# Kernel optimization log

Measured on AMD Instinct MI355X. Metric: run time of the kernel, lower is better.

## Reference

```python
import jax, jax.numpy as jnp
import numpy as np

HID = 1024     # hidden_dim
HEADS = 8      # num_heads
HD = HID // HEADS  # head_dim = 128
MD = 8         # manifold_dim
L = 3          # num_layers
B, S = 8, 1024
EPS = 1e-7
BALL_MAX = 1.0 - 1e-5  # clamp inside Poincare ball (|curvature| = 1)


def expmap0(v):
    """Hyperbolic exponential map at origin, curvature -1 (Poincare ball)."""
    n = jnp.sqrt(jnp.sum(v * v, axis=-1, keepdims=True))
    n = jnp.maximum(n, EPS)
    return jnp.tanh(n) * v / n


def logmap0(y):
    """Hyperbolic logarithm map at origin, curvature -1 (Poincare ball)."""
    n = jnp.sqrt(jnp.sum(y * y, axis=-1, keepdims=True))
    n_c = jnp.clip(n, EPS, BALL_MAX)
    return jnp.arctanh(n_c) * y / n_c


def setup_inputs() -> dict:
    key = jax.random.key(0)
    ks = jax.random.split(key, 6)
    sc = 0.02
    return {
        "x": jax.random.normal(ks[0], (B, S, HID), dtype=jnp.float32),
        "W_qkv": jax.random.normal(ks[1], (HID, 3 * HID), dtype=jnp.float32) * sc,
        "b_qkv": jnp.zeros((3 * HID,), dtype=jnp.float32),
        "W_pinv": jax.random.normal(ks[2], (HID, MD), dtype=jnp.float32) * sc,
        "b_pinv": jnp.zeros((MD,), dtype=jnp.float32),
        "W_attn": jax.random.normal(ks[3], (L, MD, HID), dtype=jnp.float32) * sc,
        "b_attn": jnp.zeros((L, HID), dtype=jnp.float32),
        "W_out": jax.random.normal(ks[4], (HID, HID), dtype=jnp.float32) * sc,
        "b_out": jnp.zeros((HID,), dtype=jnp.float32),
    }


def reference(x, W_qkv, b_qkv, W_pinv, b_pinv, W_attn, b_attn, W_out, b_out):
    inv_sqrt_d = 1.0 / np.sqrt(HD).astype(np.float32)
    cur = x
    for l in range(L):
        qkv = jnp.einsum('bsh,hd->bsd', cur, W_qkv) + b_qkv  # [B,S,3*HID]
        q, k, v = jnp.split(qkv, 3, axis=-1)
        # [B,S,HID] -> [B,HEADS,S,HD]
        def heads(t):
            return t.reshape(B, S, HEADS, HD).transpose(0, 2, 1, 3)
        q, k, v = heads(q), heads(k), heads(v)
        # geometric 'flow': hyperbolic retraction of Q/K onto the Poincare ball
        # (parallel transport at the origin is identity)
        qf = expmap0(q)
        kf = expmap0(k)
        scores = jnp.einsum('bhqd,bhkd->bhqk', qf, kf) * inv_sqrt_d
        att = jax.nn.softmax(scores, axis=-1)
        o = jnp.einsum('bhqk,bhkd->bhqd', att, v)  # [B,H,S,HD]
        o = o.transpose(0, 2, 1, 3).reshape(B, S, HID)
        # project to manifold coords, then per-layer pattern projection back
        m = jnp.einsum('bsh,hm->bsm', o, W_pinv) + b_pinv           # [B,S,MD]
        upd = jnp.einsum('bsm,mh->bsh', m, W_attn[l]) + b_attn[l]   # [B,S,HID]
        cur = cur + upd
    return jnp.einsum('bsh,hd->bsd', cur, W_out) + b_out
```

## Files before the change

### kernel.cpp

```cpp
#include <hip/hip_runtime.h>
#include <hip/hip_bf16.h>
#include <hip/hip_fp8.h>
#include <cstdint>

typedef __hip_bfloat16 bf16;
typedef __bf16 b8 __attribute__((ext_vector_type(8)));
typedef float f4v __attribute__((ext_vector_type(4)));
typedef short s8v __attribute__((ext_vector_type(8)));
typedef int i8v __attribute__((ext_vector_type(8)));

#define DEVI static __device__ __forceinline__

DEVI void gload16(const void* g, void* l) {
  __builtin_amdgcn_global_load_lds(
      (const __attribute__((address_space(1))) void*)(uintptr_t)g,
      (__attribute__((address_space(3))) void*)(uint32_t)(uintptr_t)l,
      16, 0, 0);
}

DEVI f4v mfma_bf16(b8 a, b8 b, f4v c) {
  return __builtin_amdgcn_mfma_f32_16x16x32_bf16(a, b, c, 0, 0, 0);
}

DEVI f4v mfma_fp8(i8v a, i8v b, f4v c) {
  return __builtin_amdgcn_mfma_scale_f32_16x16x128_f8f6f4(
      a, b, c, 0, 0, 0, 0x7F7F7F7F, 0, 0x7F7F7F7F);
}

DEVI uint8_t to_fp8(float f) {
  __hip_fp8_e4m3 v(f);
  return v.__x;
}

__global__ void prep_kernel(const float* __restrict__ x, float* __restrict__ cur,
                            bf16* __restrict__ curb, uint8_t* __restrict__ curf8) {
  int i = (blockIdx.x * 256 + threadIdx.x) * 4;
  float4 v = *(const float4*)(x + i);
  *(float4*)(cur + i) = v;
  __hip_bfloat162 a, b;
  a.x = __float2bfloat16(v.x); a.y = __float2bfloat16(v.y);
  b.x = __float2bfloat16(v.z); b.y = __float2bfloat16(v.w);
  *(__hip_bfloat162*)(curb + i) = a;
  *(__hip_bfloat162*)(curb + i + 2) = b;
  uint32_t p = (uint32_t)to_fp8(v.x) | ((uint32_t)to_fp8(v.y) << 8) |
               ((uint32_t)to_fp8(v.z) << 16) | ((uint32_t)to_fp8(v.w) << 24);
  *(uint32_t*)(curf8 + i) = p;
}

__global__ void transpose_cast(const float* __restrict__ in, bf16* __restrict__ out,
                               int R, int C) {
  __shared__ float tile[32][33];
  int c0 = blockIdx.x * 32, r0 = blockIdx.y * 32;
  int tx = threadIdx.x & 31, ty = threadIdx.x >> 5;
  for (int rr = ty; rr < 32; rr += 8)
    tile[rr][tx] = in[(size_t)(r0 + rr) * C + c0 + tx];
  __syncthreads();
  for (int cc = ty; cc < 32; cc += 8)
    out[(size_t)(c0 + cc) * R + r0 + tx] = __float2bfloat16(tile[tx][cc]);
}

__global__ void transpose_cast_fp8(const float* __restrict__ in,
                                   uint8_t* __restrict__ out, int R, int C) {
  __shared__ float tile[32][33];
  int c0 = blockIdx.x * 32, r0 = blockIdx.y * 32;
  int tx = threadIdx.x & 31, ty = threadIdx.x >> 5;
  for (int rr = ty; rr < 32; rr += 8)
    tile[rr][tx] = in[(size_t)(r0 + rr) * C + c0 + tx];
  __syncthreads();
  for (int cc = ty; cc < 32; cc += 8)
    out[(size_t)(c0 + cc) * R + r0 + tx] = to_fp8(tile[tx][cc]);
}

__global__ __launch_bounds__(256, 3)
void gemm_qkv_fp8(const uint8_t* __restrict__ A, const uint8_t* __restrict__ Bt,
                  const float* __restrict__ bias, bf16* __restrict__ Qo,
                  bf16* __restrict__ Ko, bf16* __restrict__ Vto, int M, int N,
                  int K) {
  __shared__ uint8_t As[128 * 128];
  __shared__ uint8_t Bs[128 * 128];
  __shared__ float red[2][128];
  const int t = threadIdx.x;
  const int w = t >> 6, lane = t & 63;
  const int lm = lane & 15, qd = lane >> 4;
  const int m0 = blockIdx.x * 128, n0 = blockIdx.y * 128;
  const int wm = (w & 1) * 64, wn = (w >> 1) * 64;

  const uint8_t* Ag = A + (size_t)m0 * K;
  const uint8_t* Bg = Bt + (size_t)n0 * K;

  f4v acc[4][4];
  f4v zero = {0.f, 0.f, 0.f, 0.f};
#pragma unroll
  for (int i = 0; i < 4; i++)
#pragma unroll
    for (int j = 0; j < 4; j++) acc[i][j] = zero;

  for (int k0 = 0; k0 < K; k0 += 128) {
#pragma unroll
    for (int c = 0; c < 4; c++) {
      int s = c * 256 + t;
      int r = s >> 3;
      int kc = (s & 7) ^ (r & 7);
      gload16(Ag + (size_t)r * K + k0 + kc * 16, &As[s * 16]);
      gload16(Bg + (size_t)r * K + k0 + kc * 16, &Bs[s * 16]);
    }
    __syncthreads();
    i8v af[4], bfr[4];
#pragma unroll
    for (int tm = 0; tm < 4; tm++) {
      int row = wm + tm * 16 + lm;
      int ch = (qd * 2) ^ (row & 7);
      union { int4 q[2]; i8v v; } u;
      u.q[0] = *(const int4*)&As[row * 128 + ch * 16];
      u.q[1] = *(const int4*)&As[row * 128 + (ch ^ 1) * 16];
      af[tm] = u.v;
    }
#pragma unroll
    for (int tn = 0; tn < 4; tn++) {
      int row = wn + tn * 16 + lm;
      int ch = (qd * 2) ^ (row & 7);
      union { int4 q[2]; i8v v; } u;
      u.q[0] = *(const int4*)&Bs[row * 128 + ch * 16];
      u.q[1] = *(const int4*)&Bs[row * 128 + (ch ^ 1) * 16];
      bfr[tn] = u.v;
    }
#pragma unroll
    for (int tm = 0; tm < 4; tm++)
#pragma unroll
      for (int tn = 0; tn < 4; tn++)
        acc[tm][tn] = mfma_fp8(af[tm], bfr[tn], acc[tm][tn]);
    __syncthreads();
  }

  const int part = n0 >> 10;
  const int hh = (n0 >> 7) & 7;
  if (part == 2) {
#pragma unroll
    for (int tm = 0; tm < 4; tm++)
#pragma unroll
      for (int tn = 0; tn < 4; tn++) {
        int d = wn + tn * 16 + lm;
        float bv = bias[n0 + d];
        int row0 = m0 + wm + tm * 16 + qd * 4;
        int b = row0 >> 10, s0 = row0 & 1023;
        bf16 vt[4];
#pragma unroll
        for (int r = 0; r < 4; r++) vt[r] = __float2bfloat16(acc[tm][tn][r] + bv);
        *(ushort4*)&Vto[((size_t)(b * 8 + hh)) * 131072 + (size_t)d * 1024 + s0] =
            *(ushort4*)vt;
      }
  } else {
    float bvs[4];
#pragma unroll
    for (int tn = 0; tn < 4; tn++) bvs[tn] = bias[n0 + wn + tn * 16 + lm];
    float ss[4][4];
#pragma unroll
    for (int tm = 0; tm < 4; tm++)
#pragma unroll
      for (int r = 0; r < 4; r++) {
        float s = 0.f;
#pragma unroll
        for (int tn = 0; tn < 4; tn++) {
          float v = acc[tm][tn][r] + bvs[tn];
          s += v * v;
        }
#pragma unroll
        for (int off = 1; off < 16; off <<= 1) s += __shfl_xor(s, off, 64);
        ss[tm][r] = s;
      }
    if (lm == 0) {
#pragma unroll
      for (int tm = 0; tm < 4; tm++)
#pragma unroll
        for (int r = 0; r < 4; r++)
          red[w >> 1][wm + tm * 16 + qd * 4 + r] = ss[tm][r];
    }
    __syncthreads();
    const float qsc = (part == 0) ? 0.08838834764831845f : 1.0f;
    float scr[4][4];
#pragma unroll
    for (int tm = 0; tm < 4; tm++)
#pragma unroll
      for (int r = 0; r < 4; r++) {
        int row = wm + tm * 16 + qd * 4 + r;
        float tot = red[0][row] + red[1][row];
        float nrm = fmaxf(sqrtf(tot), 1e-7f);
        scr[tm][r] = tanhf(nrm) / nrm * qsc;
      }
    bf16* dst = (part == 0) ? Qo : Ko;
#pragma unroll
    for (int tm = 0; tm < 4; tm++)
#pragma unroll
      for (int tn = 0; tn < 4; tn++) {
        int d = wn + tn * 16 + lm;
        int row0 = m0 + wm + tm * 16 + qd * 4;
        int b = row0 >> 10, s0 = row0 & 1023;
#pragma unroll
        for (int r = 0; r < 4; r++)
          dst[(((size_t)(b * 8 + hh)) * 1024 + s0 + r) * 128 + d] =
              __float2bfloat16((acc[tm][tn][r] + bvs[tn]) * scr[tm][r]);
      }
  }
}

__global__ __launch_bounds__(256, 3)
void gemm_bt(const bf16* __restrict__ A, const bf16* __restrict__ Bt,
             const float* __restrict__ bias, float* __restrict__ Cf, int M, int N,
             int K) {
  __shared__ bf16 As[128 * 64];
  __shared__ bf16 Bs[128 * 64];
  const int t = threadIdx.x;
  const int w = t >> 6, lane = t & 63;
  const int lm = lane & 15, qd = lane >> 4;
  const int m0 = blockIdx.x * 128, n0 = blockIdx.y * 128;
  const int wm = (w & 1) * 64, wn = (w >> 1) * 64;

  const bf16* Ag = A + (size_t)m0 * K;
  const bf16* Bg = Bt + (size_t)n0 * K;

  f4v acc[4][4];
  f4v zero = {0.f, 0.f, 0.f, 0.f};
#pragma unroll
  for (int i = 0; i < 4; i++)
#pragma unroll
    for (int j = 0; j < 4; j++) acc[i][j] = zero;

  for (int k0 = 0; k0 < K; k0 += 64) {
#pragma unroll
    for (int c = 0; c < 4; c++) {
      int s = c * 256 + t;
      int r = s >> 3;
      int kc = (s & 7) ^ (r & 7);
      gload16(Ag + (size_t)r * K + k0 + kc * 8, &As[s * 8]);
      gload16(Bg + (size_t)r * K + k0 + kc * 8, &Bs[s * 8]);
    }
    __syncthreads();
#pragma unroll
    for (int ks = 0; ks < 2; ks++) {
      b8 af[4], bfr[4];
#pragma unroll
      for (int tm = 0; tm < 4; tm++) {
        int row = wm + tm * 16 + lm;
        int ch = (ks * 4 + qd) ^ (row & 7);
        af[tm] = *(const b8*)&As[row * 64 + ch * 8];
      }
#pragma unroll
      for (int tn = 0; tn < 4; tn++) {
        int row = wn + tn * 16 + lm;
        int ch = (ks * 4 + qd) ^ (row & 7);
        bfr[tn] = *(const b8*)&Bs[row * 64 + ch * 8];
      }
#pragma unroll
      for (int tm = 0; tm < 4; tm++)
#pragma unroll
        for (int tn = 0; tn < 4; tn++)
          acc[tm][tn] = mfma_bf16(af[tm], bfr[tn], acc[tm][tn]);
    }
    __syncthreads();
  }

#pragma unroll
  for (int tm = 0; tm < 4; tm++)
#pragma unroll
    for (int tn = 0; tn < 4; tn++) {
      int col = n0 + wn + tn * 16 + lm;
      float bv = bias[col];
#pragma unroll
      for (int r = 0; r < 4; r++) {
        int row = m0 + wm + tm * 16 + qd * 4 + r;
        Cf[(size_t)row * N + col] = acc[tm][tn][r] + bv;
      }
    }
}

__global__ __launch_bounds__(256, 2)
void attn_kernel(const bf16* __restrict__ Qf, const bf16* __restrict__ Kf,
                 const bf16* __restrict__ Vt, bf16* __restrict__ O) {
  __shared__ bf16 smem[40960];
  bf16* Ps = smem + 32768;
  const int t = threadIdx.x, w = t >> 6, lane = t & 63;
  const int lm = lane & 15, qd = lane >> 4;
  const int bh = blockIdx.x, qt = blockIdx.y;
  const bf16* Qg = Qf + ((size_t)bh * 1024 + qt * 128) * 128;
  const bf16* Kg = Kf + (size_t)bh * 131072;
  const bf16* Vg = Vt + (size_t)bh * 131072;
  bf16* Pw = Ps + w * 2048;

  auto stage = [&](int kt, int b) {
    bf16* Ksb = smem + b * 16384;
    bf16* Vsb = Ksb + 8192;
#pragma unroll
    for (int c = 0; c < 4; c++) {
      int s = c * 256 + t;
      int r = s >> 4;
      int kc = (s & 15) ^ (r & 7);
      gload16(Kg + (size_t)(kt * 64 + r) * 128 + kc * 8, &Ksb[s * 8]);
      int rv = s >> 3;
      int kv = (s & 7) ^ (rv & 7);
      gload16(Vg + (size_t)rv * 1024 + kt * 64 + kv * 8, &Vsb[s * 8]);
    }
  };

  b8 qfr[2][4];
#pragma unroll
  for (int mt = 0; mt < 2; mt++)
#pragma unroll
    for (int ks = 0; ks < 4; ks++)
      qfr[mt][ks] =
          *(const b8*)(Qg + (size_t)(w * 32 + mt * 16 + lm) * 128 + ks * 32 + qd * 8);

  f4v o[2][8];
  f4v lacc[2];
  f4v zero = {0.f, 0.f, 0.f, 0.f};
#pragma unroll
  for (int mt = 0; mt < 2; mt++) {
    lacc[mt] = zero;
#pragma unroll
    for (int i = 0; i < 8; i++) o[mt][i] = zero;
  }
  union { s8v s; b8 b; } uo;
#pragma unroll
  for (int i = 0; i < 8; i++) uo.s[i] = 0x3F80;
  const b8 ones = uo.b;

  stage(0, 0);
  for (int kt = 0; kt < 16; kt++) {
    const int cb = kt & 1;
    if (kt < 15) {
      stage(kt + 1, cb ^ 1);
      asm volatile("s_waitcnt vmcnt(8)" ::: "memory");
    } else {
      asm volatile("s_waitcnt vmcnt(0)" ::: "memory");
    }
    __builtin_amdgcn_sched_barrier(0);
    __builtin_amdgcn_s_barrier();
    __builtin_amdgcn_sched_barrier(0);
    const bf16* Ks = smem + cb * 16384;
    const bf16* Vs = Ks + 8192;

    f4v sc[2][4];
#pragma unroll
    for (int mt = 0; mt < 2; mt++)
#pragma unroll
      for (int tn = 0; tn < 4; tn++) sc[mt][tn] = zero;
#pragma unroll
    for (int tn = 0; tn < 4; tn++) {
      int krow = tn * 16 + lm;
#pragma unroll
      for (int ks = 0; ks < 4; ks++) {
        int ch = (ks * 4 + qd) ^ (krow & 7);
        b8 kfr = *(const b8*)&Ks[krow * 128 + ch * 8];
        sc[0][tn] = mfma_bf16(qfr[0][ks], kfr, sc[0][tn]);
        sc[1][tn] = mfma_bf16(qfr[1][ks], kfr, sc[1][tn]);
      }
    }
#pragma unroll
    for (int mt = 0; mt < 2; mt++)
#pragma unroll
      for (int tn = 0; tn < 4; tn++)
#pragma unroll
        for (int r = 0; r < 4; r++) {
          int qi = mt * 16 + qd * 4 + r;
          int ch = (tn * 2 + (lm >> 3)) ^ ((qi >> 1) & 7);
          Pw[qi * 64 + ch * 8 + (lm & 7)] = __float2bfloat16(__expf(sc[mt][tn][r]));
        }

    b8 pa[2][2];
#pragma unroll
    for (int mt = 0; mt < 2; mt++)
#pragma unroll
      for (int kv2 = 0; kv2 < 2; kv2++) {
        int qi = mt * 16 + lm;
        int ch = (kv2 * 4 + qd) ^ ((lm >> 1) & 7);
        pa[mt][kv2] = *(const b8*)&Pw[qi * 64 + ch * 8];
      }
#pragma unroll
    for (int mt = 0; mt < 2; mt++)
#pragma unroll
      for (int kv2 = 0; kv2 < 2; kv2++)
        lacc[mt] = mfma_bf16(pa[mt][kv2], ones, lacc[mt]);
#pragma unroll
    for (int tnd = 0; tnd < 8; tnd++) {
      int drow = tnd * 16 + lm;
#pragma unroll
      for (int kv2 = 0; kv2 < 2; kv2++) {
        int ch = (kv2 * 4 + qd) ^ (drow & 7);
        b8 vfr = *(const b8*)&Vs[drow * 64 + ch * 8];
#pragma unroll
        for (int mt = 0; mt < 2; mt++)
          o[mt][tnd] = mfma_bf16(pa[mt][kv2], vfr, o[mt][tnd]);
      }
    }
    __builtin_amdgcn_sched_barrier(0);
    __builtin_amdgcn_s_barrier();
  }

  const int b = bh >> 3, h = bh & 7;
#pragma unroll
  for (int mt = 0; mt < 2; mt++) {
    float rinv[4];
#pragma unroll
    for (int r = 0; r < 4; r++) rinv[r] = 1.0f / lacc[mt][r];
#pragma unroll
    for (int tnd = 0; tnd < 8; tnd++) {
      int d = tnd * 16 + lm;
#pragma unroll
      for (int r = 0; r < 4; r++) {
        int sIdx = qt * 128 + w * 32 + mt * 16 + qd * 4 + r;
        O[((size_t)b * 1024 + sIdx) * 1024 + h * 128 + d] =
            __float2bfloat16(o[mt][tnd][r] * rinv[r]);
      }
    }
  }
}

__global__ __launch_bounds__(256, 4)
void update_kernel(const bf16* __restrict__ O, const float* __restrict__ Wpinv,
                   const float* __restrict__ bpinv, const float* __restrict__ Wattn,
                   const float* __restrict__ battn, float* __restrict__ cur,
                   bf16* __restrict__ curb, uint8_t* __restrict__ curf8) {
  const int t = threadIdx.x, w = t >> 6, lane = t & 63;
  const int r0 = blockIdx.x * 8 + w * 2;
  const int hb = lane * 4;

  float a0[8], a1[8];
#pragma unroll
  for (int j = 0; j < 8; j++) { a0[j] = 0.f; a1[j] = 0.f; }
#pragma unroll
  for (int c = 0; c < 4; c++) {
    const bf16* p0 = O + (size_t)r0 * 1024 + c * 256 + hb;
    bf16 t0[4], t1[4];
    *(ushort4*)t0 = *(const ushort4*)p0;
    *(ushort4*)t1 = *(const ushort4*)(p0 + 1024);
#pragma unroll
    for (int e = 0; e < 4; e++) {
      float v0 = __bfloat162float(t0[e]);
      float v1 = __bfloat162float(t1[e]);
      const float* wr = Wpinv + (size_t)(c * 256 + hb + e) * 8;
      float4 wa = *(const float4*)wr;
      float4 wb = *(const float4*)(wr + 4);
      a0[0] += v0 * wa.x; a0[1] += v0 * wa.y;
      a0[2] += v0 * wa.z; a0[3] += v0 * wa.w;
      a0[4] += v0 * wb.x; a0[5] += v0 * wb.y;
      a0[6] += v0 * wb.z; a0[7] += v0 * wb.w;
      a1[0] += v1 * wa.x; a1[1] += v1 * wa.y;
      a1[2] += v1 * wa.z; a1[3] += v1 * wa.w;
      a1[4] += v1 * wb.x; a1[5] += v1 * wb.y;
      a1[6] += v1 * wb.z; a1[7] += v1 * wb.w;
    }
  }
#pragma unroll
  for (int j = 0; j < 8; j++) {
#pragma unroll
    for (int off = 32; off; off >>= 1) {
      a0[j] += __shfl_xor(a0[j], off, 64);
      a1[j] += __shfl_xor(a1[j], off, 64);
    }
  }
#pragma unroll
  for (int j = 0; j < 8; j++) {
    float bp = bpinv[j];
    a0[j] += bp;
    a1[j] += bp;
  }

#pragma unroll
  for (int c = 0; c < 4; c++) {
    float4 bv = *(const float4*)(battn + c * 256 + hb);
    float u00 = bv.x, u01 = bv.y, u02 = bv.z, u03 = bv.w;
    float u10 = bv.x, u11 = bv.y, u12 = bv.z, u13 = bv.w;
#pragma unroll
    for (int j = 0; j < 8; j++) {
      float4 wv = *(const float4*)(Wattn + (size_t)j * 1024 + c * 256 + hb);
      u00 += a0[j] * wv.x; u01 += a0[j] * wv.y;
      u02 += a0[j] * wv.z; u03 += a0[j] * wv.w;
      u10 += a1[j] * wv.x; u11 += a1[j] * wv.y;
      u12 += a1[j] * wv.z; u13 += a1[j] * wv.w;
    }
    {
      float* cp = cur + (size_t)r0 * 1024 + c * 256 + hb;
      float4 c4 = *(float4*)cp;
      c4.x += u00; c4.y += u01; c4.z += u02; c4.w += u03;
      *(float4*)cp = c4;
      bf16 cb[4];
      cb[0] = __float2bfloat16(c4.x); cb[1] = __float2bfloat16(c4.y);
      cb[2] = __float2bfloat16(c4.z); cb[3] = __float2bfloat16(c4.w);
      *(ushort4*)(curb + (size_t)r0 * 1024 + c * 256 + hb) = *(ushort4*)cb;
      uint32_t p = (uint32_t)to_fp8(c4.x) | ((uint32_t)to_fp8(c4.y) << 8) |
                   ((uint32_t)to_fp8(c4.z) << 16) | ((uint32_t)to_fp8(c4.w) << 24);
      *(uint32_t*)(curf8 + (size_t)r0 * 1024 + c * 256 + hb) = p;
    }
    {
      float* cp = cur + (size_t)(r0 + 1) * 1024 + c * 256 + hb;
      float4 c4 = *(float4*)cp;
      c4.x += u10; c4.y += u11; c4.z += u12; c4.w += u13;
      *(float4*)cp = c4;
      bf16 cb[4];
      cb[0] = __float2bfloat16(c4.x); cb[1] = __float2bfloat16(c4.y);
      cb[2] = __float2bfloat16(c4.z); cb[3] = __float2bfloat16(c4.w);
      *(ushort4*)(curb + (size_t)(r0 + 1) * 1024 + c * 256 + hb) = *(ushort4*)cb;
      uint32_t p = (uint32_t)to_fp8(c4.x) | ((uint32_t)to_fp8(c4.y) << 8) |
                   ((uint32_t)to_fp8(c4.z) << 16) | ((uint32_t)to_fp8(c4.w) << 24);
      *(uint32_t*)(curf8 + (size_t)(r0 + 1) * 1024 + c * 256 + hb) = p;
    }
  }
}

extern "C" void kernel_launch(void* const* d_in, const int* in_sizes, int n_in,
                              void* d_out, int out_size, void* d_ws, size_t ws_size,
                              hipStream_t stream) {
  const float* x      = (const float*)d_in[0];
  const float* W_qkv  = (const float*)d_in[1];
  const float* b_qkv  = (const float*)d_in[2];
  const float* W_pinv = (const float*)d_in[3];
  const float* b_pinv = (const float*)d_in[4];
  const float* W_attn = (const float*)d_in[5];
  const float* b_attn = (const float*)d_in[6];
  const float* W_out  = (const float*)d_in[7];
  const float* b_out  = (const float*)d_in[8];

  char* ws = (char*)d_ws;
  size_t off = 0;
  auto alloc = [&](size_t bytes) -> void* {
    void* p = ws + off;
    off += (bytes + 255) & ~(size_t)255;
    return p;
  };
  float* cur     = (float*)alloc((size_t)8192 * 1024 * 4);
  bf16* curb     = (bf16*)alloc((size_t)8192 * 1024 * 2);
  uint8_t* curf8 = (uint8_t*)alloc((size_t)8192 * 1024);
  uint8_t* Wqkv8 = (uint8_t*)alloc((size_t)3072 * 1024);
  bf16* Woutt    = (bf16*)alloc((size_t)1024 * 1024 * 2);
  bf16* Q        = (bf16*)alloc((size_t)8192 * 1024 * 2);
  bf16* Kt       = (bf16*)alloc((size_t)8192 * 1024 * 2);
  bf16* Vt       = (bf16*)alloc((size_t)8192 * 1024 * 2);
  bf16* O        = (bf16*)alloc((size_t)8192 * 1024 * 2);
  (void)ws_size; (void)in_sizes; (void)n_in; (void)out_size;

  prep_kernel<<<8192, 256, 0, stream>>>(x, cur, curb, curf8);
  transpose_cast_fp8<<<dim3(96, 32), 256, 0, stream>>>(W_qkv, Wqkv8, 1024, 3072);
  transpose_cast<<<dim3(32, 32), 256, 0, stream>>>(W_out, Woutt, 1024, 1024);

  for (int l = 0; l < 3; l++) {
    gemm_qkv_fp8<<<dim3(64, 24), 256, 0, stream>>>(curf8, Wqkv8, b_qkv, Q, Kt, Vt,
                                                   8192, 3072, 1024);
    attn_kernel<<<dim3(64, 8), 256, 0, stream>>>(Q, Kt, Vt, O);
    update_kernel<<<1024, 256, 0, stream>>>(O, W_pinv, b_pinv,
                                            W_attn + (size_t)l * 8 * 1024,
                                            b_attn + (size_t)l * 1024, cur, curb,
                                            curf8);
  }
  gemm_bt<<<dim3(64, 8), 256, 0, stream>>>(curb, Woutt, b_out, (float*)d_out, 8192,
                                           1024, 1024);
}
```

Before: 516.0 us.

## Load K/V fragments directly from global memory in attention, drop LDS staging

Removes the double-buffered LDS staging of K and V tiles and the block barriers in the attention loop. Each wave now reads its K and V MFMA fragments straight from global memory (via L2/cache), and LDS is used only for the P tile. This cuts LDS footprint and synchronisation, but each of the four waves redundantly loads the same K/V data and loses the async prefetch overlap.

```diff
diff --git a/kernel.cpp b/kernel.cpp
--- a/kernel.cpp
+++ b/kernel.cpp
@@ -276,30 +276,14 @@
 __global__ __launch_bounds__(256, 2)
 void attn_kernel(const bf16* __restrict__ Qf, const bf16* __restrict__ Kf,
                  const bf16* __restrict__ Vt, bf16* __restrict__ O) {
-  __shared__ bf16 smem[40960];
-  bf16* Ps = smem + 32768;
+  __shared__ bf16 smem[8192];
   const int t = threadIdx.x, w = t >> 6, lane = t & 63;
   const int lm = lane & 15, qd = lane >> 4;
   const int bh = blockIdx.x, qt = blockIdx.y;
   const bf16* Qg = Qf + ((size_t)bh * 1024 + qt * 128) * 128;
   const bf16* Kg = Kf + (size_t)bh * 131072;
   const bf16* Vg = Vt + (size_t)bh * 131072;
-  bf16* Pw = Ps + w * 2048;
-
-  auto stage = [&](int kt, int b) {
-    bf16* Ksb = smem + b * 16384;
-    bf16* Vsb = Ksb + 8192;
-#pragma unroll
-    for (int c = 0; c < 4; c++) {
-      int s = c * 256 + t;
-      int r = s >> 4;
-      int kc = (s & 15) ^ (r & 7);
-      gload16(Kg + (size_t)(kt * 64 + r) * 128 + kc * 8, &Ksb[s * 8]);
-      int rv = s >> 3;
-      int kv = (s & 7) ^ (rv & 7);
-      gload16(Vg + (size_t)rv * 1024 + kt * 64 + kv * 8, &Vsb[s * 8]);
-    }
-  };
+  bf16* Pw = smem + w * 2048;
 
   b8 qfr[2][4];
 #pragma unroll
@@ -323,21 +307,7 @@
   for (int i = 0; i < 8; i++) uo.s[i] = 0x3F80;
   const b8 ones = uo.b;
 
-  stage(0, 0);
   for (int kt = 0; kt < 16; kt++) {
-    const int cb = kt & 1;
-    if (kt < 15) {
-      stage(kt + 1, cb ^ 1);
-      asm volatile("s_waitcnt vmcnt(8)" ::: "memory");
-    } else {
-      asm volatile("s_waitcnt vmcnt(0)" ::: "memory");
-    }
-    __builtin_amdgcn_sched_barrier(0);
-    __builtin_amdgcn_s_barrier();
-    __builtin_amdgcn_sched_barrier(0);
-    const bf16* Ks = smem + cb * 16384;
-    const bf16* Vs = Ks + 8192;
-
     f4v sc[2][4];
 #pragma unroll
     for (int mt = 0; mt < 2; mt++)
@@ -345,11 +315,10 @@
       for (int tn = 0; tn < 4; tn++) sc[mt][tn] = zero;
 #pragma unroll
     for (int tn = 0; tn < 4; tn++) {
-      int krow = tn * 16 + lm;
+      const bf16* kr = Kg + (size_t)(kt * 64 + tn * 16 + lm) * 128 + qd * 8;
 #pragma unroll
       for (int ks = 0; ks < 4; ks++) {
-        int ch = (ks * 4 + qd) ^ (krow & 7);
-        b8 kfr = *(const b8*)&Ks[krow * 128 + ch * 8];
+        b8 kfr = *(const b8*)(kr + ks * 32);
         sc[0][tn] = mfma_bf16(qfr[0][ks], kfr, sc[0][tn]);
         sc[1][tn] = mfma_bf16(qfr[1][ks], kfr, sc[1][tn]);
       }
@@ -381,18 +350,15 @@
         lacc[mt] = mfma_bf16(pa[mt][kv2], ones, lacc[mt]);
 #pragma unroll
     for (int tnd = 0; tnd < 8; tnd++) {
-      int drow = tnd * 16 + lm;
+      const bf16* vr = Vg + (size_t)(tnd * 16 + lm) * 1024 + kt * 64 + qd * 8;
 #pragma unroll
       for (int kv2 = 0; kv2 < 2; kv2++) {
-        int ch = (kv2 * 4 + qd) ^ (drow & 7);
-        b8 vfr = *(const b8*)&Vs[drow * 64 + ch * 8];
+        b8 vfr = *(const b8*)(vr + kv2 * 32);
 #pragma unroll
         for (int mt = 0; mt < 2; mt++)
           o[mt][tnd] = mfma_bf16(pa[mt][kv2], vfr, o[mt][tnd]);
       }
     }
-    __builtin_amdgcn_sched_barrier(0);
-    __builtin_amdgcn_s_barrier();
   }
 
   const int b = bh >> 3, h = bh & 7;
```

Measured after the change: 731.7 us. 1.42x slower.
